# Optimization experiments

Hardware: AMD Instinct MI355X
Metric: run time of the kernel (lower is better)

The kernel has to match this reference:

```python
import jax, jax.numpy as jnp
import numpy as np

N_NODES = 100000
HIDDEN = 128


def gcn_conv(x, edge_index, W, b, n_nodes):
    """PyG GCNConv: out = D^{-1/2} (A+I) D^{-1/2} (x @ W) + b."""
    src, dst = edge_index[0], edge_index[1]
    # add self-loops
    loop = jnp.arange(n_nodes, dtype=src.dtype)
    src = jnp.concatenate([src, loop])
    dst = jnp.concatenate([dst, loop])
    # degree of (A + I) w.r.t. destination nodes
    deg = jax.ops.segment_sum(jnp.ones_like(dst, dtype=x.dtype), dst,
                              num_segments=n_nodes)
    dinv = jax.lax.rsqrt(jnp.where(deg > 0, deg, 1.0))
    norm = dinv[src] * dinv[dst]  # [E+N]
    h = x @ W                      # [N, F_out]
    msg = h[src] * norm[:, None]   # gather + scale, [E+N, F_out]
    out = jax.ops.segment_sum(msg, dst, num_segments=n_nodes)
    return out + b


def setup_inputs() -> dict:
    key = jax.random.key(0)
    k1, k2, k3, k4, k5, k6 = jax.random.split(key, 6)
    num_features, num_classes = 128, 40
    n_edges = 1600000
    x = jax.random.normal(k1, (N_NODES, num_features), dtype=jnp.float32)
    edge_index = jax.random.randint(k2, (2, n_edges), 0, N_NODES, dtype=jnp.int64)
    s1 = 1.0 / np.sqrt(num_features)
    s2 = 1.0 / np.sqrt(HIDDEN)
    W1 = jax.random.uniform(k3, (num_features, HIDDEN), jnp.float32, -s1, s1)
    b1 = jax.random.uniform(k4, (HIDDEN,), jnp.float32, -s1, s1)
    W2 = jax.random.uniform(k5, (HIDDEN, num_classes), jnp.float32, -s2, s2)
    b2 = jax.random.uniform(k6, (num_classes,), jnp.float32, -s2, s2)
    return {"x": x, "edge_index": edge_index, "W1": W1, "b1": b1,
            "W2": W2, "b2": b2}


def reference(x, edge_index, W1, b1, W2, b2):
    n = x.shape[0]
    h = gcn_conv(x, edge_index, W1, b1, n)
    h = jax.nn.relu(h)
    # dropout is identity in eval mode (training=False)
    out = gcn_conv(h, edge_index, W2, b2, n)
    return out
```

## Files before the change

### kernel.cpp

```cpp
#include <hip/hip_runtime.h>

typedef short s16x8 __attribute__((ext_vector_type(8)));
typedef float f32x4 __attribute__((ext_vector_type(4)));


__device__ inline unsigned pack_bf16(float a, float b) {
  unsigned ua = __float_as_uint(a), ub = __float_as_uint(b);
  ua += 0x7fffu + ((ua >> 16) & 1u);
  ub += 0x7fffu + ((ub >> 16) & 1u);
  return (ua >> 16) | (ub & 0xffff0000u);
}
__device__ inline float unpack_lo(unsigned u) { return __uint_as_float(u << 16); }
__device__ inline float unpack_hi(unsigned u) { return __uint_as_float(u & 0xffff0000u); }


__global__ void kb_count(const int* __restrict__ dst, int E,
                         int* __restrict__ bucket_cnt, int NB) {
  __shared__ int h[256];
  h[threadIdx.x] = 0;
  __syncthreads();
  int i = blockIdx.x * blockDim.x + threadIdx.x;
  int stride = gridDim.x * blockDim.x;
  for (; i < E; i += stride) atomicAdd(&h[dst[i] >> 9], 1);
  __syncthreads();
  if (threadIdx.x < NB && h[threadIdx.x]) atomicAdd(&bucket_cnt[threadIdx.x], h[threadIdx.x]);
}

__global__ void kb_scan(const int* __restrict__ bucket_cnt, int NB, int E,
                        int* __restrict__ bucket_start, int* __restrict__ bucket_cursor) {
  int tid = threadIdx.x, lane = tid & 63, w = tid >> 6;
  int v = (tid < NB) ? bucket_cnt[tid] : 0;
  int x = v;
#pragma unroll
  for (int off = 1; off < 64; off <<= 1) {
    int u = __shfl_up(x, off);
    if (lane >= off) x += u;
  }
  __shared__ int ws4[4];
  if (lane == 63) ws4[w] = x;
  __syncthreads();
  int add = 0;
  for (int k = 0; k < w; ++k) add += ws4[k];
  x += add;
  int excl = x - v;
  if (tid < NB) {
    bucket_start[tid] = excl;
    bucket_cursor[tid] = excl;
  }
  if (tid == 0) bucket_start[NB] = E;
}

__global__ __launch_bounds__(256) void kb_scatter(const int* __restrict__ src,
                                                  const int* __restrict__ dst, int E,
                                                  int* __restrict__ bucket_cursor,
                                                  unsigned* __restrict__ pairs) {
  constexpr int T = 16;
  __shared__ int bin_cnt[256], bin_base[256];
  bin_cnt[threadIdx.x] = 0;
  __syncthreads();
  int base = blockIdx.x * (256 * T);
  unsigned u[T];
  int bb[T], slot[T];
#pragma unroll
  for (int t = 0; t < T; ++t) {
    int e = base + t * 256 + threadIdx.x;
    if (e < E) {
      int s = src[e], d = dst[e];
      bb[t] = d >> 9;
      u[t] = (unsigned)s | ((unsigned)(d & 511) << 17);
      slot[t] = atomicAdd(&bin_cnt[bb[t]], 1);
    } else {
      bb[t] = -1;
    }
  }
  __syncthreads();
  if (bin_cnt[threadIdx.x] > 0)
    bin_base[threadIdx.x] = atomicAdd(&bucket_cursor[threadIdx.x], bin_cnt[threadIdx.x]);
  __syncthreads();
#pragma unroll
  for (int t = 0; t < T; ++t)
    if (bb[t] >= 0) pairs[bin_base[bb[t]] + slot[t]] = u[t];
}

__global__ __launch_bounds__(256) void kc_csr(const unsigned* __restrict__ pairs,
                                              const int* __restrict__ bucket_start,
                                              int N, float* __restrict__ dinv,
                                              int* __restrict__ row_start,
                                              int* __restrict__ deg,
                                              int* __restrict__ col) {
  int b = blockIdx.x;
  int pbase = bucket_start[b], m = bucket_start[b + 1] - pbase;
  int tid = threadIdx.x, lane = tid & 63, w = tid >> 6;
  __shared__ int cnt[512], cur[512];
  __shared__ int ws4[4];
  cnt[tid] = 0;
  cnt[tid + 256] = 0;
  __syncthreads();
  for (int i = tid; i < m; i += 256) atomicAdd(&cnt[pairs[pbase + i] >> 17], 1);
  __syncthreads();
  int c0 = cnt[2 * tid], c1 = cnt[2 * tid + 1];
  int p = c0 + c1, x = p;
#pragma unroll
  for (int off = 1; off < 64; off <<= 1) {
    int uu = __shfl_up(x, off);
    if (lane >= off) x += uu;
  }
  if (lane == 63) ws4[w] = x;
  __syncthreads();
  int add = 0;
  for (int k = 0; k < w; ++k) add += ws4[k];
  x += add;
  int xe = x - p;
  cur[2 * tid] = xe;
  cur[2 * tid + 1] = xe + c0;
  int n0 = b * 512 + 2 * tid;
  if (n0 < N) {
    deg[n0] = c0;
    dinv[n0] = rsqrtf((float)(c0 + 1));
    row_start[n0] = pbase + xe;
  }
  if (n0 + 1 < N) {
    deg[n0 + 1] = c1;
    dinv[n0 + 1] = rsqrtf((float)(c1 + 1));
    row_start[n0 + 1] = pbase + xe + c0;
  }
  __syncthreads();
  for (int i = tid; i < m; i += 256) {
    unsigned uu = pairs[pbase + i];
    int pos = atomicAdd(&cur[uu >> 17], 1);
    col[pbase + pos] = (int)(uu & 131071u);
  }
}


__global__ void kw_trans(const float* __restrict__ W, int NC, int NT,
                         unsigned* __restrict__ WT) {
  int id = blockIdx.x * 256 + threadIdx.x;
  if (id >= NT * 64) return;
  int n = id >> 6, kd = id & 63;
  float a = 0.f, b = 0.f;
  if (n < NC) {
    a = W[(2 * kd) * NC + n];
    b = W[(2 * kd + 1) * NC + n];
  }
  WT[id] = pack_bf16(a, b);
}


template <int NTILES, int GSTRIDE, int NCOLS, bool A_FP32>
__global__ __launch_bounds__(256, 4) void k_gemm_mfma(const void* __restrict__ Ain,
                                                      const unsigned* __restrict__ WT,
                                                      const float* __restrict__ dinv,
                                                      unsigned* __restrict__ G, int N) {
  __shared__ unsigned Ws[NTILES * 16 * 68];
  __shared__ unsigned As[64 * 68];

  const int tid = threadIdx.x;
  const int row0 = blockIdx.x * 64;

  constexpr int WV2 = NTILES * 16 * 32;
  const uint2* WT2 = (const uint2*)WT;
#pragma unroll
  for (int i = tid; i < WV2; i += 256) {
    int r = i >> 5, kd2 = i & 31;
    *(uint2*)&Ws[r * 68 + kd2 * 2] = WT2[i];
  }

  if (A_FP32) {
    const float4* X4 = (const float4*)Ain + (size_t)row0 * 32;
#pragma unroll
    for (int i = tid; i < 2048; i += 256) {
      int r = i >> 5, c4 = i & 31;
      uint2 o = {0u, 0u};
      if (row0 + r < N) {
        float4 xv = X4[i];
        o.x = pack_bf16(xv.x, xv.y);
        o.y = pack_bf16(xv.z, xv.w);
      }
      *(uint2*)&As[r * 68 + c4 * 2] = o;
    }
  } else {
    const uint2* H2 = (const uint2*)Ain + (size_t)row0 * 32;
#pragma unroll
    for (int i = tid; i < 2048; i += 256) {
      int r = i >> 5, kd2 = i & 31;
      uint2 o = {0u, 0u};
      if (row0 + r < N) o = H2[i];
      *(uint2*)&As[r * 68 + kd2 * 2] = o;
    }
  }
  __syncthreads();

  const int w = tid >> 6, lane = tid & 63;
  const int quad = lane >> 4, n16 = lane & 15;

  f32x4 acc[NTILES];
#pragma unroll
  for (int t = 0; t < NTILES; ++t) acc[t] = {0.f, 0.f, 0.f, 0.f};

  const char* Ab = (const char*)As + (w * 16 + n16) * 272 + quad * 16;
  const char* Bb = (const char*)Ws + n16 * 272 + quad * 16;
#pragma unroll
  for (int s = 0; s < 4; ++s) {
    s16x8 a = *(const s16x8*)(Ab + s * 64);
#pragma unroll
    for (int t = 0; t < NTILES; ++t) {
      s16x8 b = *(const s16x8*)(Bb + t * 16 * 272 + s * 64);
      acc[t] = __builtin_amdgcn_mfma_f32_16x16x32_bf16(a, b, acc[t], 0, 0, 0);
    }
  }

#pragma unroll
  for (int reg = 0; reg < 4; ++reg) {
    int r = row0 + w * 16 + quad * 4 + reg;
    float dv = (r < N) ? dinv[r] : 0.f;
#pragma unroll
    for (int t = 0; t < NTILES; ++t) {
      float v = acc[t][reg] * dv;
      float vp = __shfl_xor(v, 1);
      int colc = t * 16 + n16;
      if ((n16 & 1) == 0 && colc < NCOLS && r < N)
        G[(size_t)r * GSTRIDE + t * 8 + (n16 >> 1)] = pack_bf16(v, vp);
    }
  }
}


__global__ void k_agg1(const unsigned* __restrict__ g1, const int* __restrict__ row_start,
                       const int* __restrict__ deg, const int* __restrict__ col,
                       const float* __restrict__ dinv, const float* __restrict__ b1,
                       unsigned* __restrict__ h2, int N) {
  int node = blockIdx.x * 4 + (threadIdx.x >> 6);
  if (node >= N) return;
  int lane = threadIdx.x & 63;
  unsigned su = g1[(size_t)node * 64 + lane];
  float ax = unpack_lo(su), ay = unpack_hi(su);
  int start = row_start[node], cnt = deg[node];
  int j = 0;
  for (; j + 16 <= cnt; j += 16) {
    unsigned u[16];
#pragma unroll
    for (int t = 0; t < 16; ++t)
      u[t] = g1[(size_t)col[start + j + t] * 64 + lane];
#pragma unroll
    for (int t = 0; t < 16; ++t) {
      ax += unpack_lo(u[t]);
      ay += unpack_hi(u[t]);
    }
  }
  for (; j + 8 <= cnt; j += 8) {
    unsigned u[8];
#pragma unroll
    for (int t = 0; t < 8; ++t)
      u[t] = g1[(size_t)col[start + j + t] * 64 + lane];
#pragma unroll
    for (int t = 0; t < 8; ++t) {
      ax += unpack_lo(u[t]);
      ay += unpack_hi(u[t]);
    }
  }
  for (; j + 4 <= cnt; j += 4) {
    unsigned u[4];
#pragma unroll
    for (int t = 0; t < 4; ++t)
      u[t] = g1[(size_t)col[start + j + t] * 64 + lane];
#pragma unroll
    for (int t = 0; t < 4; ++t) {
      ax += unpack_lo(u[t]);
      ay += unpack_hi(u[t]);
    }
  }
  for (; j < cnt; ++j) {
    unsigned u = g1[(size_t)col[start + j] * 64 + lane];
    ax += unpack_lo(u);
    ay += unpack_hi(u);
  }
  float dn = dinv[node];
  float2 bb = ((const float2*)b1)[lane];
  float ox = fmaxf(fmaf(ax, dn, bb.x), 0.f);
  float oy = fmaxf(fmaf(ay, dn, bb.y), 0.f);
  h2[(size_t)node * 64 + lane] = pack_bf16(ox, oy);
}


__global__ void k_agg2(const unsigned* __restrict__ g2, const int* __restrict__ row_start,
                       const int* __restrict__ deg, const int* __restrict__ col,
                       const float* __restrict__ dinv, const float* __restrict__ b2,
                       float* __restrict__ out, int N) {
  int lane = threadIdx.x & 63;
  int sub = lane / 20;
  int f = lane - sub * 20;
  int node = (blockIdx.x * 4 + (threadIdx.x >> 6)) * 3 + sub;
  if (sub >= 3 || node >= N) return;
  unsigned su = g2[(size_t)node * 20 + f];
  float ax = unpack_lo(su), ay = unpack_hi(su);
  int start = row_start[node], cnt = deg[node];
  int j = 0;
  for (; j + 8 <= cnt; j += 8) {
    unsigned u[8];
#pragma unroll
    for (int t = 0; t < 8; ++t)
      u[t] = g2[(size_t)col[start + j + t] * 20 + f];
#pragma unroll
    for (int t = 0; t < 8; ++t) {
      ax += unpack_lo(u[t]);
      ay += unpack_hi(u[t]);
    }
  }
  for (; j + 4 <= cnt; j += 4) {
    unsigned u[4];
#pragma unroll
    for (int t = 0; t < 4; ++t)
      u[t] = g2[(size_t)col[start + j + t] * 20 + f];
#pragma unroll
    for (int t = 0; t < 4; ++t) {
      ax += unpack_lo(u[t]);
      ay += unpack_hi(u[t]);
    }
  }
  for (; j < cnt; ++j) {
    unsigned u = g2[(size_t)col[start + j] * 20 + f];
    ax += unpack_lo(u);
    ay += unpack_hi(u);
  }
  float dn = dinv[node];
  float2 o;
  o.x = fmaf(ax, dn, b2[2 * f]);
  o.y = fmaf(ay, dn, b2[2 * f + 1]);
  *(float2*)&out[(size_t)node * 40 + 2 * f] = o;
}


extern "C" void kernel_launch(void* const* d_in, const int* in_sizes, int n_in,
                              void* d_out, int out_size, void* d_ws, size_t ws_size,
                              hipStream_t stream) {
  const float* x = (const float*)d_in[0];
  const int* ei = (const int*)d_in[1];
  const float* W1 = (const float*)d_in[2];
  const float* b1 = (const float*)d_in[3];
  const float* W2 = (const float*)d_in[4];
  const float* b2 = (const float*)d_in[5];

  const int F = in_sizes[3];
  const int N = in_sizes[0] / F;
  const int E = in_sizes[1] / 2;
  const int* esrc = ei;
  const int* edst = ei + E;
  const int NB = (N + 511) / 512;

  char* ws = (char*)d_ws;
  int* bucket_cnt = (int*)(ws + 0);
  int* bucket_start = (int*)(ws + 4096);
  int* bucket_cursor = (int*)(ws + 8192);
  unsigned* w1t = (unsigned*)(ws + 16384);
  unsigned* w2t = (unsigned*)(ws + 49152);
  float* dinv = (float*)(ws + 65536);
  int* row_start = (int*)(ws + 466944);
  int* deg = (int*)(ws + 868352);
  unsigned* pairs = (unsigned*)(ws + 1269760);
  int* colx = (int*)(ws + 7669760);
  unsigned* g1 = (unsigned*)(ws + 14073856);
  unsigned* h2 = (unsigned*)(ws + 39673856);
  unsigned* g2 = g1;

  hipMemsetAsync(bucket_cnt, 0, 1024, stream);

  kb_count<<<256, 256, 0, stream>>>(edst, E, bucket_cnt, NB);
  kb_scan<<<1, 256, 0, stream>>>(bucket_cnt, NB, E, bucket_start, bucket_cursor);
  kb_scatter<<<(E + 4095) / 4096, 256, 0, stream>>>(esrc, edst, E, bucket_cursor, pairs);
  kc_csr<<<NB, 256, 0, stream>>>(pairs, bucket_start, N, dinv, row_start, deg, colx);

  kw_trans<<<32, 256, 0, stream>>>(W1, 128, 128, w1t);
  kw_trans<<<12, 256, 0, stream>>>(W2, 40, 48, w2t);

  const int gblocks = (N + 63) / 64;
  k_gemm_mfma<8, 64, 128, true><<<gblocks, 256, 0, stream>>>(x, w1t, dinv, g1, N);
  k_agg1<<<(N + 3) / 4, 256, 0, stream>>>(g1, row_start, deg, colx, dinv, b1, h2, N);
  k_gemm_mfma<3, 20, 40, false><<<gblocks, 256, 0, stream>>>(h2, w2t, dinv, g2, N);
  k_agg2<<<(N + 11) / 12, 256, 0, stream>>>(g2, row_start, deg, colx, dinv, b2,
                                            (float*)d_out, N);
}
```

Before: 297.8 us.

## Rework layer-1 aggregation to gather four neighbors per wave with 16-byte loads

The layer-1 aggregation kernel now splits each 64-lane wave into four 16-lane groups. Each group fetches a different neighbor's 256-byte bf16 row with 16-byte vector loads, so each load instruction covers four neighbors. Column indices are loaded cooperatively, one per lane, and handed to the groups with shuffles instead of every lane reading them redundantly. Partial sums are reduced across groups with xor shuffles, and group 0 writes the biased, ReLU'd bf16 result. The goal is fewer memory instructions and better latency hiding, at the cost of more registers and cross-lane shuffle work.

```diff
diff --git a/kernel.cpp b/kernel.cpp
--- a/kernel.cpp
+++ b/kernel.cpp
@@ -2,6 +2,7 @@
 
 typedef short s16x8 __attribute__((ext_vector_type(8)));
 typedef float f32x4 __attribute__((ext_vector_type(4)));
+typedef float f32x2 __attribute__((ext_vector_type(2)));
 
 
 __device__ inline unsigned pack_bf16(float a, float b) {
@@ -226,60 +227,135 @@
 }
 
 
-__global__ void k_agg1(const unsigned* __restrict__ g1, const int* __restrict__ row_start,
-                       const int* __restrict__ deg, const int* __restrict__ col,
-                       const float* __restrict__ dinv, const float* __restrict__ b1,
-                       unsigned* __restrict__ h2, int N) {
+__global__ __launch_bounds__(256) void k_agg1(const unsigned* __restrict__ g1,
+                                              const int* __restrict__ row_start,
+                                              const int* __restrict__ deg,
+                                              const int* __restrict__ col,
+                                              const float* __restrict__ dinv,
+                                              const float* __restrict__ b1,
+                                              unsigned* __restrict__ h2, int N) {
   int node = blockIdx.x * 4 + (threadIdx.x >> 6);
   if (node >= N) return;
-  int lane = threadIdx.x & 63;
-  unsigned su = g1[(size_t)node * 64 + lane];
-  float ax = unpack_lo(su), ay = unpack_hi(su);
-  int start = row_start[node], cnt = deg[node];
-  int j = 0;
-  for (; j + 16 <= cnt; j += 16) {
-    unsigned u[16];
-#pragma unroll
-    for (int t = 0; t < 16; ++t)
-      u[t] = g1[(size_t)col[start + j + t] * 64 + lane];
-#pragma unroll
-    for (int t = 0; t < 16; ++t) {
-      ax += unpack_lo(u[t]);
-      ay += unpack_hi(u[t]);
-    }
-  }
-  for (; j + 8 <= cnt; j += 8) {
-    unsigned u[8];
-#pragma unroll
-    for (int t = 0; t < 8; ++t)
-      u[t] = g1[(size_t)col[start + j + t] * 64 + lane];
-#pragma unroll
-    for (int t = 0; t < 8; ++t) {
-      ax += unpack_lo(u[t]);
-      ay += unpack_hi(u[t]);
-    }
-  }
-  for (; j + 4 <= cnt; j += 4) {
-    unsigned u[4];
-#pragma unroll
-    for (int t = 0; t < 4; ++t)
-      u[t] = g1[(size_t)col[start + j + t] * 64 + lane];
-#pragma unroll
-    for (int t = 0; t < 4; ++t) {
-      ax += unpack_lo(u[t]);
-      ay += unpack_hi(u[t]);
-    }
-  }
-  for (; j < cnt; ++j) {
-    unsigned u = g1[(size_t)col[start + j] * 64 + lane];
-    ax += unpack_lo(u);
-    ay += unpack_hi(u);
-  }
-  float dn = dinv[node];
-  float2 bb = ((const float2*)b1)[lane];
-  float ox = fmaxf(fmaf(ax, dn, bb.x), 0.f);
-  float oy = fmaxf(fmaf(ay, dn, bb.y), 0.f);
-  h2[(size_t)node * 64 + lane] = pack_bf16(ox, oy);
+  const int lane = threadIdx.x & 63;
+  const int g = lane >> 4;
+  const unsigned boff = (unsigned)(lane & 15) * 16u;
+  const char* __restrict__ g1b = (const char*)g1;
+
+  f32x2 acc0 = {0.f, 0.f}, acc1 = {0.f, 0.f}, acc2 = {0.f, 0.f}, acc3 = {0.f, 0.f};
+
+#define ACC4(U)                                          \
+  acc0 += (f32x2){unpack_lo((U).x), unpack_hi((U).x)};   \
+  acc1 += (f32x2){unpack_lo((U).y), unpack_hi((U).y)};   \
+  acc2 += (f32x2){unpack_lo((U).z), unpack_hi((U).z)};   \
+  acc3 += (f32x2){unpack_lo((U).w), unpack_hi((U).w)};
+
+  if (g == 0) {
+    uint4 su = *(const uint4*)(g1b + ((((unsigned)node) << 8) | boff));
+    ACC4(su);
+  }
+
+  const int start = row_start[node], cnt = deg[node];
+  if (cnt > 0) {
+    const int last = start + cnt - 1;
+    int j = 0;
+    for (;;) {
+      int ci = start + j + lane;
+      int cv = col[ci < last ? ci : last];
+      int rem = cnt - j;
+      if (rem >= 64) {
+#pragma unroll
+        for (int s = 0; s < 16; s += 4) {
+          int c0 = __shfl(cv, s * 4 + g);
+          int c1 = __shfl(cv, s * 4 + 4 + g);
+          int c2 = __shfl(cv, s * 4 + 8 + g);
+          int c3 = __shfl(cv, s * 4 + 12 + g);
+          uint4 u0 = *(const uint4*)(g1b + ((((unsigned)c0) << 8) | boff));
+          uint4 u1 = *(const uint4*)(g1b + ((((unsigned)c1) << 8) | boff));
+          uint4 u2 = *(const uint4*)(g1b + ((((unsigned)c2) << 8) | boff));
+          uint4 u3 = *(const uint4*)(g1b + ((((unsigned)c3) << 8) | boff));
+          ACC4(u0);
+          ACC4(u1);
+          ACC4(u2);
+          ACC4(u3);
+        }
+        j += 64;
+        if (j >= cnt) break;
+        continue;
+      }
+      int fs = rem >> 2;
+      int s = 0;
+      for (; s + 4 <= fs; s += 4) {
+        int c0 = __shfl(cv, s * 4 + g);
+        int c1 = __shfl(cv, s * 4 + 4 + g);
+        int c2 = __shfl(cv, s * 4 + 8 + g);
+        int c3 = __shfl(cv, s * 4 + 12 + g);
+        uint4 u0 = *(const uint4*)(g1b + ((((unsigned)c0) << 8) | boff));
+        uint4 u1 = *(const uint4*)(g1b + ((((unsigned)c1) << 8) | boff));
+        uint4 u2 = *(const uint4*)(g1b + ((((unsigned)c2) << 8) | boff));
+        uint4 u3 = *(const uint4*)(g1b + ((((unsigned)c3) << 8) | boff));
+        ACC4(u0);
+        ACC4(u1);
+        ACC4(u2);
+        ACC4(u3);
+      }
+      if (s + 2 <= fs) {
+        int c0 = __shfl(cv, s * 4 + g);
+        int c1 = __shfl(cv, s * 4 + 4 + g);
+        uint4 u0 = *(const uint4*)(g1b + ((((unsigned)c0) << 8) | boff));
+        uint4 u1 = *(const uint4*)(g1b + ((((unsigned)c1) << 8) | boff));
+        ACC4(u0);
+        ACC4(u1);
+        s += 2;
+      }
+      if (s < fs) {
+        int c0 = __shfl(cv, s * 4 + g);
+        uint4 u0 = *(const uint4*)(g1b + ((((unsigned)c0) << 8) | boff));
+        ACC4(u0);
+        ++s;
+      }
+      int pr = rem & 3;
+      int cpr = __shfl(cv, fs * 4 + g);
+      if (g < pr) {
+        uint4 u0 = *(const uint4*)(g1b + ((((unsigned)cpr) << 8) | boff));
+        ACC4(u0);
+      }
+      break;
+    }
+  }
+#undef ACC4
+
+  acc0.x += __shfl_xor(acc0.x, 16);
+  acc0.y += __shfl_xor(acc0.y, 16);
+  acc1.x += __shfl_xor(acc1.x, 16);
+  acc1.y += __shfl_xor(acc1.y, 16);
+  acc2.x += __shfl_xor(acc2.x, 16);
+  acc2.y += __shfl_xor(acc2.y, 16);
+  acc3.x += __shfl_xor(acc3.x, 16);
+  acc3.y += __shfl_xor(acc3.y, 16);
+  acc0.x += __shfl_xor(acc0.x, 32);
+  acc0.y += __shfl_xor(acc0.y, 32);
+  acc1.x += __shfl_xor(acc1.x, 32);
+  acc1.y += __shfl_xor(acc1.y, 32);
+  acc2.x += __shfl_xor(acc2.x, 32);
+  acc2.y += __shfl_xor(acc2.y, 32);
+  acc3.x += __shfl_xor(acc3.x, 32);
+  acc3.y += __shfl_xor(acc3.y, 32);
+
+  if (g == 0) {
+    float dn = dinv[node];
+    int r4 = (lane & 15) * 4;
+    const float2* bp = (const float2*)b1;
+    float2 bb0 = bp[r4 + 0];
+    float2 bb1 = bp[r4 + 1];
+    float2 bb2 = bp[r4 + 2];
+    float2 bb3 = bp[r4 + 3];
+    uint4 o;
+    o.x = pack_bf16(fmaxf(fmaf(acc0.x, dn, bb0.x), 0.f), fmaxf(fmaf(acc0.y, dn, bb0.y), 0.f));
+    o.y = pack_bf16(fmaxf(fmaf(acc1.x, dn, bb1.x), 0.f), fmaxf(fmaf(acc1.y, dn, bb1.y), 0.f));
+    o.z = pack_bf16(fmaxf(fmaf(acc2.x, dn, bb2.x), 0.f), fmaxf(fmaf(acc2.y, dn, bb2.y), 0.f));
+    o.w = pack_bf16(fmaxf(fmaf(acc3.x, dn, bb3.x), 0.f), fmaxf(fmaf(acc3.y, dn, bb3.y), 0.f));
+    *(uint4*)(h2 + (size_t)node * 64 + r4) = o;
+  }
 }
 
 
```

Result: no change. 294.1 us (-1.2%).

## Store layer-1 features in column slices so aggregation gathers fit in cache

Applied to the files above, without the earlier changes.

The first GEMM now writes its bf16 output split into 8 feature slices of 16 columns, each stored contiguously across all nodes. The first aggregation kernel runs one block group per slice, and each pair of lanes gathers a 32-byte neighbor row with 16-byte vector loads. Each block handles 128 nodes, with two lanes per node. The aim is to keep each slice's working set (about 3.2 MB) resident in cache during the random neighbor gathers, and to use wider loads. In exchange, the column index lists are read 8 times, each gathered row is a small 32-byte access, and the deeper unroll paths were removed.

```diff
diff --git a/kernel.cpp b/kernel.cpp
--- a/kernel.cpp
+++ b/kernel.cpp
@@ -2,6 +2,7 @@
 
 typedef short s16x8 __attribute__((ext_vector_type(8)));
 typedef float f32x4 __attribute__((ext_vector_type(4)));
+typedef float f32x2 __attribute__((ext_vector_type(2)));
 
 
 __device__ inline unsigned pack_bf16(float a, float b) {
@@ -147,7 +148,7 @@
 }
 
 
-template <int NTILES, int GSTRIDE, int NCOLS, bool A_FP32>
+template <int NTILES, int GSTRIDE, int NCOLS, bool A_FP32, bool SLICED>
 __global__ __launch_bounds__(256, 4) void k_gemm_mfma(const void* __restrict__ Ain,
                                                       const unsigned* __restrict__ WT,
                                                       const float* __restrict__ dinv,
@@ -219,67 +220,76 @@
       float v = acc[t][reg] * dv;
       float vp = __shfl_xor(v, 1);
       int colc = t * 16 + n16;
-      if ((n16 & 1) == 0 && colc < NCOLS && r < N)
-        G[(size_t)r * GSTRIDE + t * 8 + (n16 >> 1)] = pack_bf16(v, vp);
-    }
-  }
-}
-
-
-__global__ void k_agg1(const unsigned* __restrict__ g1, const int* __restrict__ row_start,
-                       const int* __restrict__ deg, const int* __restrict__ col,
-                       const float* __restrict__ dinv, const float* __restrict__ b1,
-                       unsigned* __restrict__ h2, int N) {
-  int node = blockIdx.x * 4 + (threadIdx.x >> 6);
+      if ((n16 & 1) == 0 && colc < NCOLS && r < N) {
+        size_t addr = SLICED ? ((size_t)t * (size_t)N + (size_t)r) * 8 + (n16 >> 1)
+                             : (size_t)r * GSTRIDE + t * 8 + (n16 >> 1);
+        G[addr] = pack_bf16(v, vp);
+      }
+    }
+  }
+}
+
+
+__global__ __launch_bounds__(256) void k_agg1(const unsigned* __restrict__ g1s,
+                                              const int* __restrict__ row_start,
+                                              const int* __restrict__ deg,
+                                              const int* __restrict__ col,
+                                              const float* __restrict__ dinv,
+                                              const float* __restrict__ b1,
+                                              unsigned* __restrict__ h2, int N) {
+  const int s = blockIdx.x & 7;
+  const int chunk = blockIdx.x >> 3;
+  const int lane = threadIdx.x & 63;
+  const int wv = threadIdx.x >> 6;
+  const int p = lane >> 1, h = lane & 1;
+  const int node = chunk * 128 + wv * 32 + p;
   if (node >= N) return;
-  int lane = threadIdx.x & 63;
-  unsigned su = g1[(size_t)node * 64 + lane];
-  float ax = unpack_lo(su), ay = unpack_hi(su);
-  int start = row_start[node], cnt = deg[node];
+  const unsigned hb = (unsigned)h << 4;
+  const char* __restrict__ sb = (const char*)g1s + (size_t)s * (size_t)N * 32u;
+
+  f32x2 a0 = {0.f, 0.f}, a1 = {0.f, 0.f}, a2 = {0.f, 0.f}, a3 = {0.f, 0.f};
+
+#define ACC4(U)                                         \
+  a0 += (f32x2){unpack_lo((U).x), unpack_hi((U).x)};    \
+  a1 += (f32x2){unpack_lo((U).y), unpack_hi((U).y)};    \
+  a2 += (f32x2){unpack_lo((U).z), unpack_hi((U).z)};    \
+  a3 += (f32x2){unpack_lo((U).w), unpack_hi((U).w)};
+
+  {
+    uint4 su = *(const uint4*)(sb + ((((unsigned)node) << 5) | hb));
+    ACC4(su);
+  }
+
+  const int start = row_start[node], cnt = deg[node];
+  const int* __restrict__ cp = col + start;
   int j = 0;
-  for (; j + 16 <= cnt; j += 16) {
-    unsigned u[16];
-#pragma unroll
-    for (int t = 0; t < 16; ++t)
-      u[t] = g1[(size_t)col[start + j + t] * 64 + lane];
-#pragma unroll
-    for (int t = 0; t < 16; ++t) {
-      ax += unpack_lo(u[t]);
-      ay += unpack_hi(u[t]);
-    }
-  }
-  for (; j + 8 <= cnt; j += 8) {
-    unsigned u[8];
-#pragma unroll
-    for (int t = 0; t < 8; ++t)
-      u[t] = g1[(size_t)col[start + j + t] * 64 + lane];
-#pragma unroll
-    for (int t = 0; t < 8; ++t) {
-      ax += unpack_lo(u[t]);
-      ay += unpack_hi(u[t]);
-    }
-  }
   for (; j + 4 <= cnt; j += 4) {
-    unsigned u[4];
-#pragma unroll
-    for (int t = 0; t < 4; ++t)
-      u[t] = g1[(size_t)col[start + j + t] * 64 + lane];
-#pragma unroll
-    for (int t = 0; t < 4; ++t) {
-      ax += unpack_lo(u[t]);
-      ay += unpack_hi(u[t]);
-    }
+    int c0 = cp[j], c1 = cp[j + 1], c2 = cp[j + 2], c3 = cp[j + 3];
+    uint4 u0 = *(const uint4*)(sb + ((((unsigned)c0) << 5) | hb));
+    uint4 u1 = *(const uint4*)(sb + ((((unsigned)c1) << 5) | hb));
+    uint4 u2 = *(const uint4*)(sb + ((((unsigned)c2) << 5) | hb));
+    uint4 u3 = *(const uint4*)(sb + ((((unsigned)c3) << 5) | hb));
+    ACC4(u0);
+    ACC4(u1);
+    ACC4(u2);
+    ACC4(u3);
   }
   for (; j < cnt; ++j) {
-    unsigned u = g1[(size_t)col[start + j] * 64 + lane];
-    ax += unpack_lo(u);
-    ay += unpack_hi(u);
-  }
-  float dn = dinv[node];
-  float2 bb = ((const float2*)b1)[lane];
-  float ox = fmaxf(fmaf(ax, dn, bb.x), 0.f);
-  float oy = fmaxf(fmaf(ay, dn, bb.y), 0.f);
-  h2[(size_t)node * 64 + lane] = pack_bf16(ox, oy);
+    int c = cp[j];
+    uint4 u = *(const uint4*)(sb + ((((unsigned)c) << 5) | hb));
+    ACC4(u);
+  }
+#undef ACC4
+
+  const float dn = dinv[node];
+  const float2* __restrict__ bp = (const float2*)b1 + (s * 8 + h * 4);
+  float2 b0 = bp[0], b1v = bp[1], b2v = bp[2], b3v = bp[3];
+  uint4 o;
+  o.x = pack_bf16(fmaxf(fmaf(a0.x, dn, b0.x), 0.f), fmaxf(fmaf(a0.y, dn, b0.y), 0.f));
+  o.y = pack_bf16(fmaxf(fmaf(a1.x, dn, b1v.x), 0.f), fmaxf(fmaf(a1.y, dn, b1v.y), 0.f));
+  o.z = pack_bf16(fmaxf(fmaf(a2.x, dn, b2v.x), 0.f), fmaxf(fmaf(a2.y, dn, b2v.y), 0.f));
+  o.w = pack_bf16(fmaxf(fmaf(a3.x, dn, b3v.x), 0.f), fmaxf(fmaf(a3.y, dn, b3v.y), 0.f));
+  *(uint4*)(h2 + (size_t)node * 64 + s * 8 + h * 4) = o;
 }
 
 
@@ -374,9 +384,10 @@
   kw_trans<<<12, 256, 0, stream>>>(W2, 40, 48, w2t);
 
   const int gblocks = (N + 63) / 64;
-  k_gemm_mfma<8, 64, 128, true><<<gblocks, 256, 0, stream>>>(x, w1t, dinv, g1, N);
-  k_agg1<<<(N + 3) / 4, 256, 0, stream>>>(g1, row_start, deg, colx, dinv, b1, h2, N);
-  k_gemm_mfma<3, 20, 40, false><<<gblocks, 256, 0, stream>>>(h2, w2t, dinv, g2, N);
+  k_gemm_mfma<8, 64, 128, true, true><<<gblocks, 256, 0, stream>>>(x, w1t, dinv, g1, N);
+  const int chunks = (N + 127) / 128;
+  k_agg1<<<chunks * 8, 256, 0, stream>>>(g1, row_start, deg, colx, dinv, b1, h2, N);
+  k_gemm_mfma<3, 20, 40, false, false><<<gblocks, 256, 0, stream>>>(h2, w2t, dinv, g2, N);
   k_agg2<<<(N + 11) / 12, 256, 0, stream>>>(g2, row_start, deg, colx, dinv, b2,
                                             (float*)d_out, N);
 }
```

After: 325.8 us. 1.09x slower.
